# Kernel tuning notes

Hardware: AMD Instinct MI355X
Metric: run time of the kernel (lower is better)

## Reference

```python
import jax, jax.numpy as jnp
import numpy as np

N = 20000      # nodes
E = 320000     # edges (avg degree 16)
DIN = 512
DOUT = 512


def setup_inputs() -> dict:
    key = jax.random.key(0)
    ks = jax.random.split(key, 20)
    inp = {}
    inp["X"] = jax.random.normal(ks[0], (N, DIN), jnp.float32)
    inp["edge_index"] = jax.random.randint(ks[1], (2, E), 0, N)
    inp["edge_weight"] = jax.random.uniform(ks[2], (E,), jnp.float32, minval=0.1, maxval=1.0)
    inp["H"] = jax.random.normal(ks[3], (N, DOUT), jnp.float32)
    # six GCNConv layers: x-convs [DIN,DOUT], h-convs [DOUT,DOUT], each with bias [DOUT]
    specs = [("xz", DIN), ("hz", DOUT), ("xr", DIN), ("hr", DOUT), ("xh", DIN), ("hh", DOUT)]
    for i, (tag, din) in enumerate(specs):
        inp[f"W_{tag}"] = jax.random.normal(ks[4 + 2 * i], (din, DOUT), jnp.float32) * 0.05
        inp[f"b_{tag}"] = jax.random.normal(ks[5 + 2 * i], (DOUT,), jnp.float32) * 0.01
    return inp


def _gcn_norm(edge_index, edge_weight, n):
    # PyG gcn_norm: add self-loops (weight 1), symmetric D^-1/2 A D^-1/2
    row, col = edge_index[0], edge_index[1]
    loop = jnp.arange(n, dtype=row.dtype)
    row = jnp.concatenate([row, loop])
    col = jnp.concatenate([col, loop])
    w = jnp.concatenate([edge_weight, jnp.ones((n,), edge_weight.dtype)])
    deg = jax.ops.segment_sum(w, col, num_segments=n)
    dinv = jnp.where(deg > 0, jax.lax.rsqrt(jnp.where(deg > 0, deg, 1.0)), 0.0)
    norm = dinv[row] * w * dinv[col]
    return row, col, norm


def _gcn_conv(x, W, b, row, col, norm, n):
    # out[i] = sum_{j->i} norm_e * (x W)[j] + b
    xw = x @ W                               # [N, DOUT] dense GEMM
    msg = norm[:, None] * xw[row]            # [E+N, DOUT] gather
    return jax.ops.segment_sum(msg, col, num_segments=n) + b


def reference(X, edge_index, edge_weight, H,
              W_xz, b_xz, W_hz, b_hz,
              W_xr, b_xr, W_hr, b_hr,
              W_xh, b_xh, W_hh, b_hh):
    n = X.shape[0]
    row, col, norm = _gcn_norm(edge_index, edge_weight, n)
    conv = lambda x, W, b: _gcn_conv(x, W, b, row, col, norm, n)
    Z = jax.nn.sigmoid(conv(X, W_xz, b_xz) + conv(H, W_hz, b_hz))
    R = jax.nn.sigmoid(conv(X, W_xr, b_xr) + conv(H, W_hr, b_hr))
    H_tilde = jnp.tanh(conv(X, W_xh, b_xh) + conv(H * R, W_hh, b_hh))
    return Z * H + (1.0 - Z) * H_tilde
```

## Files before the change

### kernel.cpp

```cpp
#include <hip/hip_runtime.h>

#define NN 20000
#define NP 20096
#define NE 320000
#define DD 512

typedef __bf16 bf16x8 __attribute__((ext_vector_type(8)));
typedef float f32x4 __attribute__((ext_vector_type(4)));
typedef float f32x2 __attribute__((ext_vector_type(2)));
typedef unsigned short u16;

__device__ __forceinline__ float sigmoidf_(float x) { return 1.f / (1.f + expf(-x)); }

__device__ __forceinline__ unsigned bf16pair(float a, float b) {
  unsigned ua = __builtin_bit_cast(unsigned, a);
  unsigned ub = __builtin_bit_cast(unsigned, b);
  ua = (ua + 0x7FFFu + ((ua >> 16) & 1u)) >> 16;
  ub = (ub + 0x7FFFu + ((ub >> 16) & 1u)) >> 16;
  return ua | (ub << 16);
}
__device__ __forceinline__ u16 bf16one(float a) {
  unsigned ua = __builtin_bit_cast(unsigned, a);
  return (u16)((ua + 0x7FFFu + ((ua >> 16) & 1u)) >> 16);
}
__device__ __forceinline__ float bflo(unsigned w) { return __builtin_bit_cast(float, w << 16); }
__device__ __forceinline__ float bfhi(unsigned w) { return __builtin_bit_cast(float, w & 0xFFFF0000u); }
__device__ __forceinline__ float bf2f(u16 v) { return __builtin_bit_cast(float, (unsigned)v << 16); }

__device__ __forceinline__ void gload16(const void* g, void* l) {
  __builtin_amdgcn_global_load_lds(
      (const __attribute__((address_space(1))) unsigned int*)g,
      (__attribute__((address_space(3))) unsigned int*)l, 16, 0, 0);
}

#define CVT_B 10000
#define INIT_B 79
#define WT_B 1536
__global__ __launch_bounds__(256) void k_setup(
    const float* __restrict__ X, const float* __restrict__ H,
    u16* __restrict__ Xb, u16* __restrict__ Hb,
    const float* __restrict__ W0, const float* __restrict__ W1,
    const float* __restrict__ W2, const float* __restrict__ W3,
    const float* __restrict__ W4, const float* __restrict__ W5,
    u16* __restrict__ T, float* __restrict__ deg, int* __restrict__ cnt) {
  __shared__ float t[32][33];
  int b = blockIdx.x;
  if (b < CVT_B) {
    const int n8 = NN * DD / 8;
    int i = b * 256 + threadIdx.x;
    const float* src = (i < n8) ? X : H;
    u16* dst = (i < n8) ? Xb : Hb;
    int k = (i < n8) ? i : i - n8;
    const float4* s = (const float4*)src;
    float4 v0 = s[k * 2], v1 = s[k * 2 + 1];
    uint4 o = {bf16pair(v0.x, v0.y), bf16pair(v0.z, v0.w),
               bf16pair(v1.x, v1.y), bf16pair(v1.z, v1.w)};
    ((uint4*)dst)[k] = o;
  } else if (b < CVT_B + INIT_B) {
    int i = (b - CVT_B) * 256 + threadIdx.x;
    if (i < NN) { deg[i] = 1.0f; cnt[i] = 0; }
  } else {
    int wb = b - CVT_B - INIT_B;
    const float* Wsrc;
    switch (wb >> 8) {
      case 0: Wsrc = W0; break; case 1: Wsrc = W1; break; case 2: Wsrc = W2; break;
      case 3: Wsrc = W3; break; case 4: Wsrc = W4; break; default: Wsrc = W5; break;
    }
    u16* Wt = T + (size_t)(wb >> 8) * 262144;
    int rb = wb & 255;
    int kb = (rb & 15) * 32, nb = (rb >> 4) * 32;
    int tx = threadIdx.x & 31, ty = threadIdx.x >> 5;
#pragma unroll
    for (int i2 = 0; i2 < 4; ++i2)
      t[ty * 4 + i2][tx] = Wsrc[(size_t)(kb + ty * 4 + i2) * 512 + nb + tx];
    __syncthreads();
#pragma unroll
    for (int i2 = 0; i2 < 4; ++i2)
      Wt[(size_t)(nb + ty * 4 + i2) * 512 + kb + tx] = bf16one(t[tx][ty * 4 + i2]);
  }
}

__global__ void k_accum(const int* col, const float* w, float* deg, int* cnt) {
  int e = blockIdx.x * 256 + threadIdx.x;
  if (e < NE) {
    int c = col[e];
    atomicAdd(&deg[c], w[e]);
    atomicAdd(&cnt[c], 1);
  }
}

__global__ void k_scan(const int* cnt, int* ptr, int* pos) {
  __shared__ int sdata[1024];
  const int ITEMS = (NN + 1023) / 1024;
  int tid = threadIdx.x;
  int base = tid * ITEMS;
  int s = 0;
  for (int j = 0; j < ITEMS; ++j) { int i = base + j; if (i < NN) s += cnt[i]; }
  sdata[tid] = s;
  __syncthreads();
  for (int off = 1; off < 1024; off <<= 1) {
    int v = 0;
    if (tid >= off) v = sdata[tid - off];
    __syncthreads();
    sdata[tid] += v;
    __syncthreads();
  }
  int run = (tid == 0) ? 0 : sdata[tid - 1];
  for (int j = 0; j < ITEMS; ++j) {
    int i = base + j;
    if (i < NN) { ptr[i] = run; pos[i] = run; run += cnt[i]; }
  }
  if (tid == 0) ptr[NN] = NE;
}

__global__ void k_scatter(const int* row, const int* col, const float* w, const float* deg,
                          int* pos, int* erow, float* enorm) {
  int e = blockIdx.x * 256 + threadIdx.x;
  if (e < NE) {
    int r = row[e], c = col[e];
    int slot = atomicAdd(&pos[c], 1);
    erow[slot] = r;
    enorm[slot] = rsqrtf(deg[r]) * w[e] * rsqrtf(deg[c]);
  }
}

__global__ __launch_bounds__(256) void k_agg_dual_s2(const u16* __restrict__ Xb,
                                                     const u16* __restrict__ Hb,
                                                     const int* __restrict__ ptr,
                                                     const int* __restrict__ erow,
                                                     const float* __restrict__ enorm,
                                                     const float* __restrict__ deg,
                                                     u16* __restrict__ AXb,
                                                     u16* __restrict__ AHb) {
  int bid = blockIdx.x;
  int slice = bid & 7, nb = bid >> 3;
  int w = threadIdx.x >> 6, lane = threadIdx.x & 63;
  int node = nb * 4 + w;
  int g = lane >> 3, cl = lane & 7;
  int soff = slice * 8 + cl;
  const uint4* X4 = (const uint4*)Xb;
  const uint4* H4 = (const uint4*)Hb;
  float s = rsqrtf(deg[node]), s2 = s * s;
  int pe = ptr[node];
  int items = ptr[node + 1] - pe + 1;

  f32x2 ax[4] = {}, ah[4] = {};
  auto accum = [&](float nm, uint4 xv, uint4 hv) {
    unsigned xw[4] = {xv.x, xv.y, xv.z, xv.w};
    unsigned hw[4] = {hv.x, hv.y, hv.z, hv.w};
    f32x2 nm2 = {nm, nm};
#pragma unroll
    for (int j = 0; j < 4; ++j) {
      f32x2 xf = {bflo(xw[j]), bfhi(xw[j])};
      f32x2 hf = {bflo(hw[j]), bfhi(hw[j])};
      ax[j] += nm2 * xf;
      ah[j] += nm2 * hf;
    }
  };

  int it = g;
  for (; it + 8 < items; it += 16) {
    int rA = node; float nA = s2;
    if (it > 0) { rA = erow[pe + it - 1]; nA = enorm[pe + it - 1]; }
    int eB = pe + it + 7;
    int rB = erow[eB]; float nB = enorm[eB];
    uint4 xA = X4[(size_t)rA * 64 + soff];
    uint4 hA = H4[(size_t)rA * 64 + soff];
    uint4 xB = X4[(size_t)rB * 64 + soff];
    uint4 hB = H4[(size_t)rB * 64 + soff];
    accum(nA, xA, hA);
    accum(nB, xB, hB);
  }
  if (it < items) {
    int rA = node; float nA = s2;
    if (it > 0) { rA = erow[pe + it - 1]; nA = enorm[pe + it - 1]; }
    accum(nA, X4[(size_t)rA * 64 + soff], H4[(size_t)rA * 64 + soff]);
  }

#pragma unroll
  for (int st = 8; st < 64; st <<= 1) {
#pragma unroll
    for (int j = 0; j < 4; ++j) {
      ax[j].x += __shfl_xor(ax[j].x, st, 64); ax[j].y += __shfl_xor(ax[j].y, st, 64);
      ah[j].x += __shfl_xor(ah[j].x, st, 64); ah[j].y += __shfl_xor(ah[j].y, st, 64);
    }
  }

  if (g == 0) {
    uint4 ox = {bf16pair(ax[0].x, ax[0].y), bf16pair(ax[1].x, ax[1].y),
                bf16pair(ax[2].x, ax[2].y), bf16pair(ax[3].x, ax[3].y)};
    ((uint4*)AXb)[(size_t)node * 64 + soff] = ox;
  } else if (g == 1) {
    uint4 oh = {bf16pair(ah[0].x, ah[0].y), bf16pair(ah[1].x, ah[1].y),
                bf16pair(ah[2].x, ah[2].y), bf16pair(ah[3].x, ah[3].y)};
    ((uint4*)AHb)[(size_t)node * 64 + soff] = oh;
  }
}

__global__ __launch_bounds__(256) void k_agg_single_s2(const u16* __restrict__ Sb,
                                                       const int* __restrict__ ptr,
                                                       const int* __restrict__ erow,
                                                       const float* __restrict__ enorm,
                                                       const float* __restrict__ deg,
                                                       u16* __restrict__ Ab) {
  int bid = blockIdx.x;
  int slice = bid & 7, nb = bid >> 3;
  int w = threadIdx.x >> 6, lane = threadIdx.x & 63;
  int node = nb * 4 + w;
  int g = lane >> 3, cl = lane & 7;
  int soff = slice * 8 + cl;
  const uint4* S4 = (const uint4*)Sb;
  float s = rsqrtf(deg[node]), s2 = s * s;
  int pe = ptr[node];
  int items = ptr[node + 1] - pe + 1;

  f32x2 ax[4] = {};
  auto accum = [&](float nm, uint4 xv) {
    unsigned xw[4] = {xv.x, xv.y, xv.z, xv.w};
    f32x2 nm2 = {nm, nm};
#pragma unroll
    for (int j = 0; j < 4; ++j) {
      f32x2 xf = {bflo(xw[j]), bfhi(xw[j])};
      ax[j] += nm2 * xf;
    }
  };

  int it = g;
  for (; it + 8 < items; it += 16) {
    int rA = node; float nA = s2;
    if (it > 0) { rA = erow[pe + it - 1]; nA = enorm[pe + it - 1]; }
    int eB = pe + it + 7;
    int rB = erow[eB]; float nB = enorm[eB];
    uint4 xA = S4[(size_t)rA * 64 + soff];
    uint4 xB = S4[(size_t)rB * 64 + soff];
    accum(nA, xA);
    accum(nB, xB);
  }
  if (it < items) {
    int rA = node; float nA = s2;
    if (it > 0) { rA = erow[pe + it - 1]; nA = enorm[pe + it - 1]; }
    accum(nA, S4[(size_t)rA * 64 + soff]);
  }

#pragma unroll
  for (int st = 8; st < 64; st <<= 1) {
#pragma unroll
    for (int j = 0; j < 4; ++j) {
      ax[j].x += __shfl_xor(ax[j].x, st, 64); ax[j].y += __shfl_xor(ax[j].y, st, 64);
    }
  }

  if (g == 0) {
    uint4 ox = {bf16pair(ax[0].x, ax[0].y), bf16pair(ax[1].x, ax[1].y),
                bf16pair(ax[2].x, ax[2].y), bf16pair(ax[3].x, ax[3].y)};
    ((uint4*)Ab)[(size_t)node * 64 + soff] = ox;
  }
}

__global__ __launch_bounds__(256) void k_gemm_big(
    const u16* __restrict__ AXb, const u16* __restrict__ AHb,
    const u16* __restrict__ WtAll,
    const float* __restrict__ bxz, const float* __restrict__ bhz,
    const float* __restrict__ bxr, const float* __restrict__ bhr,
    const u16* __restrict__ Hb,
    u16* __restrict__ Zb, u16* __restrict__ HRb) {
  __shared__ unsigned char smem[32768];
  const int tid = threadIdx.x;
  const int lane = tid & 63, w = tid >> 6;
  const int wr = w >> 1, wc = w & 1;

  const int q = 157;
  const int xcd = blockIdx.x & 7, ii = blockIdx.x >> 3;
  const int wk = xcd * q + ii;
  const int rowBase = (wk >> 3) * 128;
  const int c = wk & 7;
  const int seg = c >> 2;
  const int colBase = (c & 3) * 128;

  const u16* W1 = WtAll + (size_t)(seg ? 2 : 0) * 262144;
  const u16* W2 = WtAll + (size_t)(seg ? 3 : 1) * 262144;

  f32x4 acc[4][4] = {};

  const int lrow = lane & 15;
  const int lkb = (lane >> 4) << 4;
  const int swz = (lane & 7) << 4;
  const int srow = w * 32 + (lane >> 3);
  const int scol = (((lane & 7) ^ (lane >> 3)) << 4);

  for (int pass = 0; pass < 2; ++pass) {
    const u16* A = pass ? AHb : AXb;
    const u16* Wt = pass ? W2 : W1;
    const char* Abase = (const char*)A + (size_t)(rowBase + srow) * 1024 + scol;
    const char* Bbase = (const char*)Wt + (size_t)(colBase + srow) * 1024 + scol;
    for (int k0 = 0; k0 < 512; k0 += 64) {
      __syncthreads();
#pragma unroll
      for (int t = 0; t < 4; ++t) {
        gload16(Abase + (size_t)t * 8192 + k0 * 2, &smem[w * 4096 + t * 1024]);
        gload16(Bbase + (size_t)t * 8192 + k0 * 2, &smem[16384 + w * 4096 + t * 1024]);
      }
      __syncthreads();
#pragma unroll
      for (int ks = 0; ks < 2; ++ks) {
        bf16x8 af[4], bfr[4];
#pragma unroll
        for (int fm = 0; fm < 4; ++fm) {
          int row = wr * 64 + fm * 16 + lrow;
          af[fm] = *(const bf16x8*)&smem[row * 128 + (((ks << 6) + lkb) ^ swz)];
        }
#pragma unroll
        for (int fn = 0; fn < 4; ++fn) {
          int row = wc * 64 + fn * 16 + lrow;
          bfr[fn] = *(const bf16x8*)&smem[16384 + row * 128 + (((ks << 6) + lkb) ^ swz)];
        }
#pragma unroll
        for (int fm = 0; fm < 4; ++fm)
#pragma unroll
          for (int fn = 0; fn < 4; ++fn)
            acc[fm][fn] = __builtin_amdgcn_mfma_f32_16x16x32_bf16(af[fm], bfr[fn], acc[fm][fn], 0, 0, 0);
      }
    }
  }
#pragma unroll
  for (int fm = 0; fm < 4; ++fm) {
    int rbase = rowBase + wr * 64 + fm * 16 + ((lane >> 4) << 2);
#pragma unroll
    for (int fn = 0; fn < 4; ++fn) {
      int col = colBase + wc * 64 + fn * 16 + lrow;
      float bb = seg ? (bxr[col] + bhr[col]) : (bxz[col] + bhz[col]);
#pragma unroll
      for (int r = 0; r < 4; ++r) {
        int row = rbase + r;
        if (row >= NN) continue;
        size_t idx = (size_t)row * 512 + col;
        float a = acc[fm][fn][r] + bb;
        if (seg == 0) {
          Zb[idx] = bf16one(sigmoidf_(a));
        } else {
          HRb[idx] = bf16one(bf2f(Hb[idx]) * sigmoidf_(a));
        }
      }
    }
  }
}

__global__ __launch_bounds__(256) void k_gemm_fin(
    const u16* __restrict__ AHRb, const u16* __restrict__ AXb,
    const u16* __restrict__ WtAll,
    const float* __restrict__ bxh, const float* __restrict__ bhh,
    const u16* __restrict__ Hb, const u16* __restrict__ Zb,
    float* __restrict__ out) {
  __shared__ unsigned char smem[32768];
  const int tid = threadIdx.x;
  const int lane = tid & 63, w = tid >> 6;
  const int wr = w >> 1, wc = w & 1;

  const int q = 78, r8 = 4;
  const int xcd = blockIdx.x & 7, ii = blockIdx.x >> 3;
  const int start = (xcd < r8) ? xcd * (q + 1) : r8 * (q + 1) + (xcd - r8) * q;
  const int wk = start + ii;
  const int rowBase = (wk >> 2) * 128;
  const int colBase = (wk & 3) * 128;

  f32x4 acc[4][4] = {};

  const int lrow = lane & 15;
  const int lkb = (lane >> 4) << 4;
  const int swz = (lane & 7) << 4;
  const int srow = w * 32 + (lane >> 3);
  const int scol = (((lane & 7) ^ (lane >> 3)) << 4);

  for (int pass = 0; pass < 2; ++pass) {
    const u16* A  = pass ? AXb : AHRb;
    const u16* Wt = WtAll + (size_t)(pass ? 4 : 5) * 262144;
    const char* Abase = (const char*)A + (size_t)(rowBase + srow) * 1024 + scol;
    const char* Bbase = (const char*)Wt + (size_t)(colBase + srow) * 1024 + scol;
    for (int k0 = 0; k0 < 512; k0 += 64) {
      __syncthreads();
#pragma unroll
      for (int t = 0; t < 4; ++t) {
        gload16(Abase + (size_t)t * 8192 + k0 * 2, &smem[w * 4096 + t * 1024]);
        gload16(Bbase + (size_t)t * 8192 + k0 * 2, &smem[16384 + w * 4096 + t * 1024]);
      }
      __syncthreads();
#pragma unroll
      for (int ks = 0; ks < 2; ++ks) {
        bf16x8 af[4], bfr[4];
#pragma unroll
        for (int fm = 0; fm < 4; ++fm) {
          int row = wr * 64 + fm * 16 + lrow;
          af[fm] = *(const bf16x8*)&smem[row * 128 + (((ks << 6) + lkb) ^ swz)];
        }
#pragma unroll
        for (int fn = 0; fn < 4; ++fn) {
          int row = wc * 64 + fn * 16 + lrow;
          bfr[fn] = *(const bf16x8*)&smem[16384 + row * 128 + (((ks << 6) + lkb) ^ swz)];
        }
#pragma unroll
        for (int fm = 0; fm < 4; ++fm)
#pragma unroll
          for (int fn = 0; fn < 4; ++fn)
            acc[fm][fn] = __builtin_amdgcn_mfma_f32_16x16x32_bf16(af[fm], bfr[fn], acc[fm][fn], 0, 0, 0);
      }
    }
  }
#pragma unroll
  for (int fm = 0; fm < 4; ++fm) {
    int rbase = rowBase + wr * 64 + fm * 16 + ((lane >> 4) << 2);
#pragma unroll
    for (int fn = 0; fn < 4; ++fn) {
      int col = colBase + wc * 64 + fn * 16 + lrow;
      float bb = bxh[col] + bhh[col];
#pragma unroll
      for (int r = 0; r < 4; ++r) {
        int row = rbase + r;
        if (row >= NN) continue;
        size_t idx = (size_t)row * 512 + col;
        float t = tanhf(acc[fm][fn][r] + bb);
        float z = bf2f(Zb[idx]);
        float h = bf2f(Hb[idx]);
        out[idx] = z * h + (1.f - z) * t;
      }
    }
  }
}

extern "C" void kernel_launch(void* const* d_in, const int* in_sizes, int n_in,
                              void* d_out, int out_size, void* d_ws, size_t ws_size,
                              hipStream_t stream) {
  const float* X   = (const float*)d_in[0];
  const int*   ei  = (const int*)d_in[1];
  const float* ew  = (const float*)d_in[2];
  const float* H   = (const float*)d_in[3];
  const float* Wxz = (const float*)d_in[4];  const float* bxz = (const float*)d_in[5];
  const float* Whz = (const float*)d_in[6];  const float* bhz = (const float*)d_in[7];
  const float* Wxr = (const float*)d_in[8];  const float* bxr = (const float*)d_in[9];
  const float* Whr = (const float*)d_in[10]; const float* bhr = (const float*)d_in[11];
  const float* Wxh = (const float*)d_in[12]; const float* bxh = (const float*)d_in[13];
  const float* Whh = (const float*)d_in[14]; const float* bhh = (const float*)d_in[15];
  const int* row = ei;
  const int* col = ei + NE;
  float* out = (float*)d_out;

  char* base = (char*)d_ws;
  size_t o = 0;
  auto alloc = [&](size_t b) { char* p = base + o; o += (b + 255) & ~(size_t)255; return p; };
  u16* Xb   = (u16*)alloc((size_t)NP * DD * 2);
  u16* Hb   = (u16*)alloc((size_t)NP * DD * 2);
  u16* AXb  = (u16*)alloc((size_t)NP * DD * 2);
  u16* AHb  = (u16*)alloc((size_t)NP * DD * 2);
  u16* HRb  = (u16*)alloc((size_t)NP * DD * 2);
  u16* Zb   = (u16*)alloc((size_t)NP * DD * 2);
  u16* WtAll= (u16*)alloc((size_t)6 * 512 * 512 * 2);
  float* deg  = (float*)alloc(NN * 4);
  int*   cnt  = (int*)alloc(NN * 4);
  int*   ptr  = (int*)alloc((NN + 1) * 4);
  int*   pos  = (int*)alloc(NN * 4);
  int*   erow = (int*)alloc(NE * 4);
  float* enorm= (float*)alloc(NE * 4);
  u16* AHRb = Xb;

  dim3 b256(256);
  int gE = (NE + 255) / 256;

  k_setup<<<CVT_B + INIT_B + WT_B, b256, 0, stream>>>(
      X, H, Xb, Hb, Wxz, Whz, Wxr, Whr, Wxh, Whh, WtAll, deg, cnt);

  k_accum<<<gE, b256, 0, stream>>>(col, ew, deg, cnt);
  k_scan<<<1, 1024, 0, stream>>>(cnt, ptr, pos);
  k_scatter<<<gE, b256, 0, stream>>>(row, col, ew, deg, pos, erow, enorm);

  k_agg_dual_s2<<<40000, b256, 0, stream>>>(Xb, Hb, ptr, erow, enorm, deg, AXb, AHb);

  k_gemm_big<<<1256, b256, 0, stream>>>(AXb, AHb, WtAll, bxz, bhz, bxr, bhr,
                                        Hb, Zb, HRb);

  k_agg_single_s2<<<40000, b256, 0, stream>>>(HRb, ptr, erow, enorm, deg, AHRb);

  k_gemm_fin<<<628, b256, 0, stream>>>(AHRb, AXb, WtAll, bxh, bhh,
                                       Hb, Zb, out);
}
```

Measured before the change: 385.1 us.

## Map four nodes per wavefront in aggregation kernels with 16-lane groups

The aggregation kernels now give each node a 16-lane group instead of a full 64-lane wavefront, so each wave handles four nodes. Grid size drops to match. With average degree around 17, the old 8-way edge split left many lanes idle, and the 16-lane mapping is meant to keep more lanes busy while cutting shuffle-reduction steps from three to one. The cost is less memory-level parallelism per node and more divergence between the four nodes sharing a wave when their degrees differ.

```diff
diff --git a/kernel.cpp b/kernel.cpp
--- a/kernel.cpp
+++ b/kernel.cpp
@@ -124,7 +124,7 @@
   }
 }
 
-__global__ __launch_bounds__(256) void k_agg_dual_s2(const u16* __restrict__ Xb,
+__global__ __launch_bounds__(256) void k_agg_dual_s3(const u16* __restrict__ Xb,
                                                      const u16* __restrict__ Hb,
                                                      const int* __restrict__ ptr,
                                                      const int* __restrict__ erow,
@@ -135,8 +135,9 @@
   int bid = blockIdx.x;
   int slice = bid & 7, nb = bid >> 3;
   int w = threadIdx.x >> 6, lane = threadIdx.x & 63;
-  int node = nb * 4 + w;
-  int g = lane >> 3, cl = lane & 7;
+  int node = nb * 16 + w * 4 + (lane >> 4);
+  int q = lane & 15;
+  int g = q >> 3, cl = q & 7;
   int soff = slice * 8 + cl;
   const uint4* X4 = (const uint4*)Xb;
   const uint4* H4 = (const uint4*)Hb;
@@ -159,10 +160,10 @@
   };
 
   int it = g;
-  for (; it + 8 < items; it += 16) {
+  for (; it + 2 < items; it += 4) {
     int rA = node; float nA = s2;
     if (it > 0) { rA = erow[pe + it - 1]; nA = enorm[pe + it - 1]; }
-    int eB = pe + it + 7;
+    int eB = pe + it + 1;
     int rB = erow[eB]; float nB = enorm[eB];
     uint4 xA = X4[(size_t)rA * 64 + soff];
     uint4 hA = H4[(size_t)rA * 64 + soff];
@@ -178,26 +179,23 @@
   }
 
 #pragma unroll
-  for (int st = 8; st < 64; st <<= 1) {
-#pragma unroll
-    for (int j = 0; j < 4; ++j) {
-      ax[j].x += __shfl_xor(ax[j].x, st, 64); ax[j].y += __shfl_xor(ax[j].y, st, 64);
-      ah[j].x += __shfl_xor(ah[j].x, st, 64); ah[j].y += __shfl_xor(ah[j].y, st, 64);
-    }
+  for (int j = 0; j < 4; ++j) {
+    ax[j].x += __shfl_xor(ax[j].x, 8, 64); ax[j].y += __shfl_xor(ax[j].y, 8, 64);
+    ah[j].x += __shfl_xor(ah[j].x, 8, 64); ah[j].y += __shfl_xor(ah[j].y, 8, 64);
   }
 
   if (g == 0) {
     uint4 ox = {bf16pair(ax[0].x, ax[0].y), bf16pair(ax[1].x, ax[1].y),
                 bf16pair(ax[2].x, ax[2].y), bf16pair(ax[3].x, ax[3].y)};
     ((uint4*)AXb)[(size_t)node * 64 + soff] = ox;
-  } else if (g == 1) {
+  } else {
     uint4 oh = {bf16pair(ah[0].x, ah[0].y), bf16pair(ah[1].x, ah[1].y),
                 bf16pair(ah[2].x, ah[2].y), bf16pair(ah[3].x, ah[3].y)};
     ((uint4*)AHb)[(size_t)node * 64 + soff] = oh;
   }
 }
 
-__global__ __launch_bounds__(256) void k_agg_single_s2(const u16* __restrict__ Sb,
+__global__ __launch_bounds__(256) void k_agg_single_s3(const u16* __restrict__ Sb,
                                                        const int* __restrict__ ptr,
                                                        const int* __restrict__ erow,
                                                        const float* __restrict__ enorm,
@@ -206,8 +204,9 @@
   int bid = blockIdx.x;
   int slice = bid & 7, nb = bid >> 3;
   int w = threadIdx.x >> 6, lane = threadIdx.x & 63;
-  int node = nb * 4 + w;
-  int g = lane >> 3, cl = lane & 7;
+  int node = nb * 16 + w * 4 + (lane >> 4);
+  int q = lane & 15;
+  int g = q >> 3, cl = q & 7;
   int soff = slice * 8 + cl;
   const uint4* S4 = (const uint4*)Sb;
   float s = rsqrtf(deg[node]), s2 = s * s;
@@ -226,10 +225,10 @@
   };
 
   int it = g;
-  for (; it + 8 < items; it += 16) {
+  for (; it + 2 < items; it += 4) {
     int rA = node; float nA = s2;
     if (it > 0) { rA = erow[pe + it - 1]; nA = enorm[pe + it - 1]; }
-    int eB = pe + it + 7;
+    int eB = pe + it + 1;
     int rB = erow[eB]; float nB = enorm[eB];
     uint4 xA = S4[(size_t)rA * 64 + soff];
     uint4 xB = S4[(size_t)rB * 64 + soff];
@@ -243,11 +242,8 @@
   }
 
 #pragma unroll
-  for (int st = 8; st < 64; st <<= 1) {
-#pragma unroll
-    for (int j = 0; j < 4; ++j) {
-      ax[j].x += __shfl_xor(ax[j].x, st, 64); ax[j].y += __shfl_xor(ax[j].y, st, 64);
-    }
+  for (int j = 0; j < 4; ++j) {
+    ax[j].x += __shfl_xor(ax[j].x, 8, 64); ax[j].y += __shfl_xor(ax[j].y, 8, 64);
   }
 
   if (g == 0) {
@@ -471,12 +467,12 @@
   k_scan<<<1, 1024, 0, stream>>>(cnt, ptr, pos);
   k_scatter<<<gE, b256, 0, stream>>>(row, col, ew, deg, pos, erow, enorm);
 
-  k_agg_dual_s2<<<40000, b256, 0, stream>>>(Xb, Hb, ptr, erow, enorm, deg, AXb, AHb);
+  k_agg_dual_s3<<<10000, b256, 0, stream>>>(Xb, Hb, ptr, erow, enorm, deg, AXb, AHb);
 
   k_gemm_big<<<1256, b256, 0, stream>>>(AXb, AHb, WtAll, bxz, bhz, bxr, bhr,
                                         Hb, Zb, HRb);
 
-  k_agg_single_s2<<<40000, b256, 0, stream>>>(HRb, ptr, erow, enorm, deg, AHRb);
+  k_agg_single_s3<<<10000, b256, 0, stream>>>(HRb, ptr, erow, enorm, deg, AHRb);
 
   k_gemm_fin<<<628, b256, 0, stream>>>(AHRb, AXb, WtAll, bxh, bhh,
                                        Hb, Zb, out);
```

Result: faster. 339.5 us (-11.8%).
